# Kernel optimization log

Measured on AMD Instinct MI355X. Metric: run time of the kernel, lower is better.

The kernel has to match this reference:

```python
import jax, jax.numpy as jnp
import numpy as np

N = 100000      # num_nodes
D = 128         # emb_size
LYR = 3         # num_layers
E = 1600000     # num edges (avg degree 16)
Q = 100000      # num label pairs to score


def setup_inputs() -> dict:
    key = jax.random.key(0)
    ks = jax.random.split(key, 8)
    xavier = float(np.sqrt(6.0 / (D + D)))  # xavier_uniform bound for square Linear
    return {
        "edge_index": jax.random.randint(ks[0], (2, E), 0, N),
        "edge_label_index": jax.random.randint(ks[1], (2, Q), 0, N),
        "edge_weight": jax.random.uniform(ks[2], (E,), dtype=jnp.float32),
        "emb": jax.random.uniform(ks[3], (N, D), dtype=jnp.float32, minval=-xavier, maxval=xavier),
        "gc_w": jax.random.uniform(ks[4], (LYR, D, D), dtype=jnp.float32, minval=-xavier, maxval=xavier),
        "gc_b": jnp.zeros((LYR, D), dtype=jnp.float32),
        "bi_w": jax.random.uniform(ks[5], (LYR, D, D), dtype=jnp.float32, minval=-xavier, maxval=xavier),
        "bi_b": jnp.zeros((LYR, D), dtype=jnp.float32),
        "num_nodes": N,
    }


def _get_embedding(edge_index, edge_weight, emb, gc_w, gc_b, bi_w, bi_b, num_nodes):
    row, col = edge_index[0], edge_index[1]
    ego = emb                      # [N, D]
    all_embs = [ego]
    for i in range(gc_w.shape[0]):
        # sparse adj @ ego: out[row] += w * ego[col]
        msg = jax.ops.segment_sum(edge_weight[:, None] * ego[col], row,
                                  num_segments=num_nodes)          # [N, D]
        aggr = msg @ gc_w[i].T + gc_b[i]                            # Linear (torch: x @ W.T + b)
        bi = (ego * msg) @ bi_w[i].T + bi_b[i]
        ego = jax.nn.leaky_relu(aggr + bi, negative_slope=0.2)      # eval mode: dropout = identity
        norm = ego / jnp.maximum(
            jnp.linalg.norm(ego, axis=1, keepdims=True), 1e-12)    # F.normalize(p=2, dim=1)
        all_embs.append(norm)
    return jnp.concatenate(all_embs, axis=1)                        # [N, (L+1)*D]


def reference(edge_index, edge_label_index, edge_weight, emb, gc_w, gc_b, bi_w, bi_b, num_nodes):
    all_embs = _get_embedding(edge_index, edge_weight, emb, gc_w, gc_b, bi_w, bi_b, num_nodes)
    out_src = all_embs[edge_label_index[0]]   # [Q, (L+1)*D]
    out_dst = all_embs[edge_label_index[1]]
    return jnp.sum(out_src * out_dst, axis=-1)  # [Q]
```

## Files before the change

kernel.cpp:

```cpp
#include <hip/hip_runtime.h>

#define DD 128
#define K2 256
#define NBMAX 1024
#define COLMASK 0x01FFFFFF
#define SCAP 4096

typedef short short8 __attribute__((ext_vector_type(8)));
typedef float f32x4  __attribute__((ext_vector_type(4)));

static inline size_t align256(size_t x){ return (x + 255) & ~(size_t)255; }

__device__ __forceinline__ unsigned short f2bf(float x){
  unsigned int u = __builtin_bit_cast(unsigned int, x);
  u += 0x7fff + ((u >> 16) & 1);
  return (unsigned short)(u >> 16);
}
__device__ __forceinline__ float bf2f(unsigned short h){
  unsigned int u = ((unsigned int)h) << 16;
  return __builtin_bit_cast(float, u);
}

__device__ __forceinline__ short8 prod8(short8 mv, short8 ev){
  short8 r;
#pragma unroll
  for (int u = 0; u < 8; u++){
    float p = bf2f((unsigned short)mv[u]) * bf2f((unsigned short)ev[u]);
    r[u] = (short)f2bf(p);
  }
  return r;
}

__global__ __launch_bounds__(256) void bucket_hist_kernel(
    const int* __restrict__ ei, int E, int* __restrict__ bcnt, int NB){
  __shared__ int lh[NBMAX];
  int t = threadIdx.x;
  int base = blockIdx.x * 8192;
  for (int j = t; j < NB; j += 256) lh[j] = 0;
  __syncthreads();
#pragma unroll
  for (int i = 0; i < 32; i++){
    int e = base + i*256 + t;
    if (e < E) atomicAdd(&lh[ei[e] >> 7], 1);
  }
  __syncthreads();
  for (int j = t; j < NB; j += 256){
    int c = lh[j];
    if (c) atomicAdd(&bcnt[j], c);
  }
}

__global__ __launch_bounds__(1024) void bucket_scan_kernel(
    const int* __restrict__ bcnt, int* __restrict__ bbase, int* __restrict__ bcur, int NB){
  __shared__ int a[NBMAX], btmp[NBMAX];
  int t = threadIdx.x;
  a[t] = (t < NB) ? bcnt[t] : 0;
  __syncthreads();
  int* src = a; int* dst = btmp;
  for (int o = 1; o < 1024; o <<= 1){
    int val = src[t];
    if (t >= o) val += src[t - o];
    dst[t] = val;
    __syncthreads();
    int* tm = src; src = dst; dst = tm;
  }
  int excl = (t == 0) ? 0 : src[t-1];
  if (t < NB){ bbase[t] = excl; bcur[t] = excl; }
}

__global__ __launch_bounds__(256) void fill_binned_kernel(
    const int* __restrict__ ei, const float* __restrict__ ew, int E,
    int* __restrict__ bcur, int2* __restrict__ csre, int NB){
  __shared__ int lhist[NBMAX];
  __shared__ int lbase[NBMAX];
  int t = threadIdx.x;
  int base = blockIdx.x * 4096;
  for (int j = t; j < NB; j += 256) lhist[j] = 0;
  __syncthreads();
  int rows[16];
#pragma unroll
  for (int i = 0; i < 16; i++){
    int e = base + i*256 + t;
    int r = (e < E) ? ei[e] : -1;
    rows[i] = r;
    if (r >= 0) atomicAdd(&lhist[r >> 7], 1);
  }
  __syncthreads();
  for (int j = t; j < NB; j += 256){
    int c = lhist[j];
    lbase[j] = c ? atomicAdd(&bcur[j], c) : 0;
    lhist[j] = 0;
  }
  __syncthreads();
#pragma unroll
  for (int i = 0; i < 16; i++){
    int e = base + i*256 + t;
    int r = rows[i];
    if (r >= 0){
      int b = r >> 7;
      int pos = lbase[b] + atomicAdd(&lhist[b], 1);
      int col = ei[E + e];
      float w = ew[e];
      csre[pos] = make_int2(((r & 127) << 25) | col, __float_as_int(w));
    }
  }
}

__global__ __launch_bounds__(256) void bucket_rowdeg_kernel(
    const int* __restrict__ bbase, const int* __restrict__ bcur,
    const int2* __restrict__ csre, int* __restrict__ deg, int* __restrict__ psum, int N){
  __shared__ int lc[128];
  __shared__ int red[128];
  int b = blockIdx.x, t = threadIdx.x;
  if (t < 128) lc[t] = 0;
  __syncthreads();
  int beg = bbase[b], end = bcur[b];
  for (int i = beg + t; i < end; i += 256)
    atomicAdd(&lc[((unsigned int)csre[i].x) >> 25], 1);
  __syncthreads();
  int gr = b*128 + t;
  int d = 0;
  if (t < 128 && gr < N){ d = lc[t]; deg[gr] = d; }
  if (t < 128) red[t] = (d + 7) & ~7;
  __syncthreads();
  for (int o = 64; o > 0; o >>= 1){
    if (t < o) red[t] += red[t+o];
    __syncthreads();
  }
  if (t == 0) psum[b] = red[0];
}

__global__ __launch_bounds__(1024) void pscan_kernel(
    const int* __restrict__ psum, int* __restrict__ pbase, int* __restrict__ rowptrN, int NB){
  __shared__ int a[NBMAX], btmp[NBMAX];
  int t = threadIdx.x;
  a[t] = (t < NB) ? psum[t] : 0;
  __syncthreads();
  int* src = a; int* dst = btmp;
  for (int o = 1; o < 1024; o <<= 1){
    int val = src[t];
    if (t >= o) val += src[t - o];
    dst[t] = val;
    __syncthreads();
    int* tm = src; src = dst; dst = tm;
  }
  int excl = (t == 0) ? 0 : src[t-1];
  if (t < NB) pbase[t] = excl;
  if (t == NB-1) *rowptrN = excl + psum[t];
}

__global__ __launch_bounds__(256) void sortbkt_kernel(
    const int* __restrict__ pbase, const int* __restrict__ bbase, const int* __restrict__ bcur,
    const int* __restrict__ deg, const int2* __restrict__ csre, int2* __restrict__ csre2,
    int* __restrict__ rowptr, int N){
  __shared__ int2 obuf[SCAP];
  __shared__ int lrp[129];
  __shared__ int lcur[128];
  __shared__ int sa[128], sb[128];
  int b = blockIdx.x;
  int t = threadIdx.x;
  int r0 = b*128;
  int gr = r0 + t;
  int d = (t < 128 && gr < N) ? deg[gr] : 0;
  if (t < 128){ sa[t] = (d + 7) & ~7; lcur[t] = 0; }
  __syncthreads();
  int* s0 = sa; int* s1 = sb;
  for (int o = 1; o < 128; o <<= 1){
    if (t < 128){
      int v = s0[t];
      if (t >= o) v += s0[t - o];
      s1[t] = v;
    }
    __syncthreads();
    int* tm = s0; s0 = s1; s1 = tm;
  }
  int pb = pbase[b];
  if (t < 128){
    int excl = t ? s0[t-1] : 0;
    lrp[t] = pb + excl;
    if (gr < N) rowptr[gr] = pb + excl;
    if (t == 127) lrp[128] = pb + s0[127];
  }
  __syncthreads();

  int gb = lrp[0];
  int outLen = lrp[128] - gb;
  int beg = bbase[b], bend = bcur[b];
  const int2 pad = make_int2(0, 0);

  if (outLen <= SCAP){
    for (int i = beg + t; i < bend; i += 256){
      int2 e = csre[i];
      int rl = ((unsigned int)e.x) >> 25;
      int pos = lrp[rl] - gb + atomicAdd(&lcur[rl], 1);
      obuf[pos] = e;
    }
    if (t < 128 && gr < N){
      int pbg = lrp[t] - gb + d, pe = lrp[t+1] - gb;
      for (int i = pbg; i < pe; i++) obuf[i] = pad;
    }
    __syncthreads();
    for (int i = t; i < outLen; i += 256) csre2[gb + i] = obuf[i];
  } else {
    for (int i = beg + t; i < bend; i += 256){
      int2 e = csre[i];
      int rl = ((unsigned int)e.x) >> 25;
      int pos = lrp[rl] + atomicAdd(&lcur[rl], 1);
      csre2[pos] = e;
    }
    __syncthreads();
    if (t < 128 && gr < N){
      int pbeg = lrp[t] + lcur[t];
      int pend = lrp[t+1];
      for (int i = pbeg; i < pend; i++) csre2[i] = pad;
    }
  }
}

__global__ void pack_cvt_kernel(const float* __restrict__ gcw, const float* __restrict__ biw,
                                unsigned short* __restrict__ wb, int LYR,
                                const float* __restrict__ emb, unsigned int* __restrict__ feat4u,
                                int n2, int fsU){
  int i = blockIdx.x*blockDim.x + threadIdx.x;
  int wtotal = LYR*DD*K2;
  if (i < wtotal){
    int l = i / (DD*K2);
    int r = i - l*(DD*K2);
    int n = r >> 8;
    int k = r & (K2-1);
    float v = (k < DD) ? gcw[(size_t)l*DD*DD + n*DD + k]
                       : biw[(size_t)l*DD*DD + n*DD + (k - DD)];
    wb[i] = f2bf(v);
    return;
  }
  int j = i - wtotal;
  if (j < n2){
    float2 v = *(const float2*)(emb + (size_t)j*2);
    int n = j >> 6, c = j & 63;
    feat4u[(size_t)n*fsU + c] = (unsigned int)f2bf(v.x) | ((unsigned int)f2bf(v.y) << 16);
  }
}

__global__ void gather_kernel(const int* __restrict__ rowptr, const int2* __restrict__ csre,
                              const unsigned short* __restrict__ feat, int fs,
                              unsigned int* __restrict__ msgh, int N){
  int wid = (int)(((size_t)blockIdx.x*blockDim.x + threadIdx.x) >> 6);
  int lane = threadIdx.x & 63;
  if (wid >= N) return;
  int beg = rowptr[wid], end = rowptr[wid+1];
  float ax = 0.f, ay = 0.f;
  int k = beg;
  for (; k + 16 <= end; k += 16){
    int2 e[16]; unsigned int v[16];
#pragma unroll
    for (int u = 0; u < 16; u++) e[u] = csre[k+u];
#pragma unroll
    for (int u = 0; u < 16; u++)
      v[u] = *(const unsigned int*)(feat + (size_t)(e[u].x & COLMASK)*fs + lane*2);
#pragma unroll
    for (int u = 0; u < 16; u++){
      float w = __int_as_float(e[u].y);
      ax = fmaf(w, bf2f((unsigned short)v[u]), ax);
      ay = fmaf(w, bf2f((unsigned short)(v[u]>>16)), ay);
    }
  }
  for (; k < end; k += 8){
    int2 e[8]; unsigned int v[8];
#pragma unroll
    for (int u = 0; u < 8; u++) e[u] = csre[k+u];
#pragma unroll
    for (int u = 0; u < 8; u++)
      v[u] = *(const unsigned int*)(feat + (size_t)(e[u].x & COLMASK)*fs + lane*2);
#pragma unroll
    for (int u = 0; u < 8; u++){
      float w = __int_as_float(e[u].y);
      ax = fmaf(w, bf2f((unsigned short)v[u]), ax);
      ay = fmaf(w, bf2f((unsigned short)(v[u]>>16)), ay);
    }
  }
  msgh[(size_t)wid*(DD/2) + lane] = (unsigned int)f2bf(ax) | ((unsigned int)f2bf(ay) << 16);
}

__global__ __launch_bounds__(256) void transform_mfma_kernel(
    const unsigned short* __restrict__ ego_in, const unsigned short* __restrict__ msgh,
    int fs, const unsigned short* __restrict__ wb, const float* __restrict__ gcb,
    const float* __restrict__ bib, unsigned short* __restrict__ ego_out,
    float* __restrict__ nscale, int N){
  int t = threadIdx.x;
  int wave = t >> 6, lane = t & 63;
  int m = lane & 15, q = lane >> 4;
  int wr0 = blockIdx.x * 128 + wave * 32;

  float bias[8];
#pragma unroll
  for (int ct = 0; ct < 8; ct++) bias[ct] = gcb[ct*16 + m] + bib[ct*16 + m];

  int row0 = wr0 + m, row1 = wr0 + 16 + m;
  int cr0 = row0 < N ? row0 : N-1;
  int cr1 = row1 < N ? row1 : N-1;
  const unsigned short* mrow0 = msgh   + (size_t)cr0*DD;
  const unsigned short* mrow1 = msgh   + (size_t)cr1*DD;
  const unsigned short* erow0 = ego_in + (size_t)cr0*fs;
  const unsigned short* erow1 = ego_in + (size_t)cr1*fs;
  const unsigned short* wrow  = wb + (size_t)m*K2;

  f32x4 acc[8][2];
#pragma unroll
  for (int ct = 0; ct < 8; ct++){ acc[ct][0] = (f32x4)0.f; acc[ct][1] = (f32x4)0.f; }

#pragma unroll
  for (int cc = 0; cc < 4; cc++){
    int c = cc*32 + q*8;
    short8 m0 = *(const short8*)(mrow0 + c);
    short8 m1 = *(const short8*)(mrow1 + c);
    short8 e0 = *(const short8*)(erow0 + c);
    short8 e1 = *(const short8*)(erow1 + c);
    short8 p0 = prod8(m0, e0);
    short8 p1 = prod8(m1, e1);
#pragma unroll
    for (int ct = 0; ct < 8; ct++){
      short8 bm = *(const short8*)(wrow + (size_t)ct*16*K2 + c);
      short8 bp = *(const short8*)(wrow + (size_t)ct*16*K2 + DD + c);
      acc[ct][0] = __builtin_amdgcn_mfma_f32_16x16x32_bf16(m0, bm, acc[ct][0], 0, 0, 0);
      acc[ct][1] = __builtin_amdgcn_mfma_f32_16x16x32_bf16(m1, bm, acc[ct][1], 0, 0, 0);
      acc[ct][0] = __builtin_amdgcn_mfma_f32_16x16x32_bf16(p0, bp, acc[ct][0], 0, 0, 0);
      acc[ct][1] = __builtin_amdgcn_mfma_f32_16x16x32_bf16(p1, bp, acc[ct][1], 0, 0, 0);
    }
  }

#pragma unroll
  for (int rt = 0; rt < 2; rt++){
#pragma unroll
    for (int reg = 0; reg < 4; reg++){
      int gr = wr0 + rt*16 + q*4 + reg;
      float rs = 0.f;
#pragma unroll
      for (int ct = 0; ct < 8; ct++){
        float x = acc[ct][rt][reg] + bias[ct];
        x = (x > 0.f) ? x : 0.2f*x;
        rs += x*x;
        if (gr < N) ego_out[(size_t)gr*fs + ct*16 + m] = f2bf(x);
      }
#pragma unroll
      for (int o = 1; o < 16; o <<= 1) rs += __shfl_xor(rs, o, 16);
      if (m == 0 && gr < N)
        nscale[(size_t)gr*3] = 1.0f / fmaxf(sqrtf(rs), 1e-12f);
    }
  }
}

__global__ void score_all_kernel(const int* __restrict__ eli, int Q,
                                 const unsigned int* __restrict__ feat4u, int fsU,
                                 const float* __restrict__ nsall,
                                 float* __restrict__ out){
  int wid = (int)(((size_t)blockIdx.x*blockDim.x + threadIdx.x) >> 6);
  int lane = threadIdx.x & 63;
  if (wid >= Q) return;
  int s = eli[wid];
  int d = eli[Q + wid];
  const unsigned int* sr = feat4u + (size_t)s*fsU + lane;
  const unsigned int* dr = feat4u + (size_t)d*fsU + lane;
  unsigned int a0 = sr[0],   b0 = dr[0];
  unsigned int a1 = sr[64],  b1 = dr[64];
  unsigned int a2 = sr[128], b2 = dr[128];
  unsigned int a3 = sr[192], b3 = dr[192];
  float p0 = bf2f((unsigned short)a0)*bf2f((unsigned short)b0)
           + bf2f((unsigned short)(a0>>16))*bf2f((unsigned short)(b0>>16));
  float p1 = bf2f((unsigned short)a1)*bf2f((unsigned short)b1)
           + bf2f((unsigned short)(a1>>16))*bf2f((unsigned short)(b1>>16));
  float p2 = bf2f((unsigned short)a2)*bf2f((unsigned short)b2)
           + bf2f((unsigned short)(a2>>16))*bf2f((unsigned short)(b2>>16));
  float p3 = bf2f((unsigned short)a3)*bf2f((unsigned short)b3)
           + bf2f((unsigned short)(a3>>16))*bf2f((unsigned short)(b3>>16));
  for (int o = 32; o > 0; o >>= 1){
    p0 += __shfl_xor(p0, o, 64);
    p1 += __shfl_xor(p1, o, 64);
    p2 += __shfl_xor(p2, o, 64);
    p3 += __shfl_xor(p3, o, 64);
  }
  if (lane == 0){
    const float* ss = nsall + (size_t)s*3;
    const float* ds = nsall + (size_t)d*3;
    float r = p0;
    r += p1 * ss[0] * ds[0];
    r += p2 * ss[1] * ds[1];
    r += p3 * ss[2] * ds[2];
    out[wid] = r;
  }
}

extern "C" void kernel_launch(void* const* d_in, const int* in_sizes, int n_in,
                              void* d_out, int out_size, void* d_ws, size_t ws_size,
                              hipStream_t stream){
  const int*   edge_index = (const int*)d_in[0];
  const int*   eli        = (const int*)d_in[1];
  const float* ew         = (const float*)d_in[2];
  const float* emb        = (const float*)d_in[3];
  const float* gcw        = (const float*)d_in[4];
  const float* gcb        = (const float*)d_in[5];
  const float* biw        = (const float*)d_in[6];
  const float* bib        = (const float*)d_in[7];
  const int E   = in_sizes[2];
  const int Q   = in_sizes[1] / 2;
  const int N   = in_sizes[3] / DD;
  const int LYR = in_sizes[4] / (DD*DD);
  float* out = (float*)d_out;

  const int FS  = (LYR + 1) * DD;
  const int FSU = FS / 2;

  char* base = (char*)d_ws;
  size_t off = 0;
  auto carve = [&](size_t bytes)->char*{
    char* r = base + off;
    off = align256(off + bytes);
    return r;
  };

  unsigned short* feat4  = (unsigned short*) carve((size_t)N*FS*sizeof(unsigned short));
  size_t msgB_ = (size_t)N*DD*sizeof(unsigned short);
  size_t csreB_ = (size_t)E*sizeof(int2);
  unsigned short* msgh   = (unsigned short*) carve(msgB_ > csreB_ ? msgB_ : csreB_);
  int2*           csre   = (int2*)msgh;
  unsigned short* wb     = (unsigned short*) carve((size_t)LYR*DD*K2*sizeof(unsigned short));
  float*          nsall  = (float*)          carve((size_t)3*N*sizeof(float));
  int*            rowptr = (int*)            carve((size_t)(N+1)*sizeof(int));
  int*            deg    = (int*)            carve((size_t)N*sizeof(int));
  int*            bcnt   = (int*)            carve((size_t)NBMAX*sizeof(int));
  int*            bbase  = (int*)            carve((size_t)NBMAX*sizeof(int));
  int*            bcur   = (int*)            carve((size_t)NBMAX*sizeof(int));
  int*            psum   = (int*)            carve((size_t)NBMAX*sizeof(int));
  int*            pbase  = (int*)            carve((size_t)NBMAX*sizeof(int));
  int2*           csre2  = (int2*)           carve(((size_t)E + 7*(size_t)N + 8)*sizeof(int2));
  (void)n_in; (void)out_size; (void)ws_size;

  const int NB = (N + 127)/128;

  hipMemsetAsync(bcnt, 0, (size_t)NB*sizeof(int), stream);
  bucket_hist_kernel<<<(E + 8191)/8192, 256, 0, stream>>>(edge_index, E, bcnt, NB);
  bucket_scan_kernel<<<1, 1024, 0, stream>>>(bcnt, bbase, bcur, NB);
  fill_binned_kernel<<<(E + 4095)/4096, 256, 0, stream>>>(edge_index, ew, E, bcur, csre, NB);
  bucket_rowdeg_kernel<<<NB, 256, 0, stream>>>(bbase, bcur, csre, deg, psum, N);
  pscan_kernel<<<1, 1024, 0, stream>>>(psum, pbase, rowptr + N, NB);
  sortbkt_kernel<<<NB, 256, 0, stream>>>(pbase, bbase, bcur, deg, csre, csre2, rowptr, N);
  {
    int total = LYR*DD*K2 + N*DD/2;
    pack_cvt_kernel<<<(total + 255)/256, 256, 0, stream>>>(
        gcw, biw, wb, LYR, emb, (unsigned int*)feat4, N*DD/2, FSU);
  }

  for (int l = 0; l < LYR; l++){
    int blocks = (int)(((size_t)N*64 + 255)/256);
    gather_kernel<<<blocks, 256, 0, stream>>>(rowptr, csre2, feat4 + (size_t)l*DD, FS,
                                              (unsigned int*)msgh, N);
    transform_mfma_kernel<<<(N + 127)/128, 256, 0, stream>>>(
        feat4 + (size_t)l*DD, msgh, FS, wb + (size_t)l*DD*K2,
        gcb + (size_t)l*DD, bib + (size_t)l*DD,
        feat4 + (size_t)(l+1)*DD, nsall + l, N);
  }
  {
    int blocks = (int)(((size_t)Q*64 + 255)/256);
    score_all_kernel<<<blocks, 256, 0, stream>>>(eli, Q, (const unsigned int*)feat4, FSU,
                                                 nsall, out);
  }
}
```

Baseline: 544.4 us.

## Fuse row-degree, scan and bucket sort into one kernel with atomic base

Merges the per-bucket degree count, the global prefix scan and the bucket sort into a single kernel. Each block claims its output range with an atomicAdd on a global cursor, and row ranges are stored as (begin,end) pairs instead of a rowptr array, which removes two launches and the padding of rows to multiples of 8. The gather kernel now handles non-multiple-of-8 tails with a masked final chunk. Bucket order in the CSR becomes nondeterministic, which may reduce locality, and the tail adds a little gather work per row.

```diff
diff --git a/kernel.cpp b/kernel.cpp
--- a/kernel.cpp
+++ b/kernel.cpp
@@ -106,63 +106,24 @@
   }
 }
 
-__global__ __launch_bounds__(256) void bucket_rowdeg_kernel(
+__global__ __launch_bounds__(256) void sortbkt2_kernel(
     const int* __restrict__ bbase, const int* __restrict__ bcur,
-    const int2* __restrict__ csre, int* __restrict__ deg, int* __restrict__ psum, int N){
-  __shared__ int lc[128];
-  __shared__ int red[128];
+    const int2* __restrict__ csre, int2* __restrict__ csre2,
+    int2* __restrict__ rp2, int* __restrict__ gcur, int N){
+  __shared__ int2 obuf[SCAP];
+  __shared__ int lc[128], lcur[128], lrp[128];
+  __shared__ int sa[128], sb[128];
+  __shared__ int gbase;
   int b = blockIdx.x, t = threadIdx.x;
-  if (t < 128) lc[t] = 0;
-  __syncthreads();
-  int beg = bbase[b], end = bcur[b];
-  for (int i = beg + t; i < end; i += 256)
+  int r0 = b*128;
+  if (t < 128){ lc[t] = 0; lcur[t] = 0; }
+  __syncthreads();
+  int beg = bbase[b], bend = bcur[b];
+  for (int i = beg + t; i < bend; i += 256)
     atomicAdd(&lc[((unsigned int)csre[i].x) >> 25], 1);
   __syncthreads();
-  int gr = b*128 + t;
-  int d = 0;
-  if (t < 128 && gr < N){ d = lc[t]; deg[gr] = d; }
-  if (t < 128) red[t] = (d + 7) & ~7;
-  __syncthreads();
-  for (int o = 64; o > 0; o >>= 1){
-    if (t < o) red[t] += red[t+o];
-    __syncthreads();
-  }
-  if (t == 0) psum[b] = red[0];
-}
-
-__global__ __launch_bounds__(1024) void pscan_kernel(
-    const int* __restrict__ psum, int* __restrict__ pbase, int* __restrict__ rowptrN, int NB){
-  __shared__ int a[NBMAX], btmp[NBMAX];
-  int t = threadIdx.x;
-  a[t] = (t < NB) ? psum[t] : 0;
-  __syncthreads();
-  int* src = a; int* dst = btmp;
-  for (int o = 1; o < 1024; o <<= 1){
-    int val = src[t];
-    if (t >= o) val += src[t - o];
-    dst[t] = val;
-    __syncthreads();
-    int* tm = src; src = dst; dst = tm;
-  }
-  int excl = (t == 0) ? 0 : src[t-1];
-  if (t < NB) pbase[t] = excl;
-  if (t == NB-1) *rowptrN = excl + psum[t];
-}
-
-__global__ __launch_bounds__(256) void sortbkt_kernel(
-    const int* __restrict__ pbase, const int* __restrict__ bbase, const int* __restrict__ bcur,
-    const int* __restrict__ deg, const int2* __restrict__ csre, int2* __restrict__ csre2,
-    int* __restrict__ rowptr, int N){
-  __shared__ int2 obuf[SCAP];
-  __shared__ int lrp[129];
-  __shared__ int lcur[128];
-  __shared__ int sa[128], sb[128];
-  int b = blockIdx.x;
-  int t = threadIdx.x;
-  int r0 = b*128;
-  int gr = r0 + t;
-  int d = (t < 128 && gr < N) ? deg[gr] : 0;
-  if (t < 128){ sa[t] = (d + 7) & ~7; lcur[t] = 0; }
+  int d = (t < 128) ? lc[t] : 0;
+  if (t < 128) sa[t] = d;
   __syncthreads();
   int* s0 = sa; int* s1 = sb;
   for (int o = 1; o < 128; o <<= 1){
@@ -174,45 +135,32 @@
     __syncthreads();
     int* tm = s0; s0 = s1; s1 = tm;
   }
-  int pb = pbase[b];
+  int total = s0[127];
+  if (t == 0) gbase = atomicAdd(gcur, total);
+  __syncthreads();
+  int gb = gbase;
   if (t < 128){
     int excl = t ? s0[t-1] : 0;
-    lrp[t] = pb + excl;
-    if (gr < N) rowptr[gr] = pb + excl;
-    if (t == 127) lrp[128] = pb + s0[127];
-  }
-  __syncthreads();
-
-  int gb = lrp[0];
-  int outLen = lrp[128] - gb;
-  int beg = bbase[b], bend = bcur[b];
-  const int2 pad = make_int2(0, 0);
-
-  if (outLen <= SCAP){
+    lrp[t] = excl;
+    int gr = r0 + t;
+    if (gr < N) rp2[gr] = make_int2(gb + excl, gb + excl + d);
+  }
+  __syncthreads();
+  if (total <= SCAP){
     for (int i = beg + t; i < bend; i += 256){
       int2 e = csre[i];
       int rl = ((unsigned int)e.x) >> 25;
-      int pos = lrp[rl] - gb + atomicAdd(&lcur[rl], 1);
+      int pos = lrp[rl] + atomicAdd(&lcur[rl], 1);
       obuf[pos] = e;
     }
-    if (t < 128 && gr < N){
-      int pbg = lrp[t] - gb + d, pe = lrp[t+1] - gb;
-      for (int i = pbg; i < pe; i++) obuf[i] = pad;
-    }
     __syncthreads();
-    for (int i = t; i < outLen; i += 256) csre2[gb + i] = obuf[i];
+    for (int i = t; i < total; i += 256) csre2[gb + i] = obuf[i];
   } else {
     for (int i = beg + t; i < bend; i += 256){
       int2 e = csre[i];
       int rl = ((unsigned int)e.x) >> 25;
-      int pos = lrp[rl] + atomicAdd(&lcur[rl], 1);
+      int pos = gb + lrp[rl] + atomicAdd(&lcur[rl], 1);
       csre2[pos] = e;
-    }
-    __syncthreads();
-    if (t < 128 && gr < N){
-      int pbeg = lrp[t] + lcur[t];
-      int pend = lrp[t+1];
-      for (int i = pbeg; i < pend; i++) csre2[i] = pad;
     }
   }
 }
@@ -241,13 +189,14 @@
   }
 }
 
-__global__ void gather_kernel(const int* __restrict__ rowptr, const int2* __restrict__ csre,
+__global__ void gather_kernel(const int2* __restrict__ rp2, const int2* __restrict__ csre,
                               const unsigned short* __restrict__ feat, int fs,
                               unsigned int* __restrict__ msgh, int N){
   int wid = (int)(((size_t)blockIdx.x*blockDim.x + threadIdx.x) >> 6);
   int lane = threadIdx.x & 63;
   if (wid >= N) return;
-  int beg = rowptr[wid], end = rowptr[wid+1];
+  int2 rp = rp2[wid];
+  int beg = rp.x, end = rp.y;
   float ax = 0.f, ay = 0.f;
   int k = beg;
   for (; k + 16 <= end; k += 16){
@@ -264,10 +213,31 @@
       ay = fmaf(w, bf2f((unsigned short)(v[u]>>16)), ay);
     }
   }
-  for (; k < end; k += 8){
+  for (; k + 8 <= end; k += 8){
     int2 e[8]; unsigned int v[8];
 #pragma unroll
     for (int u = 0; u < 8; u++) e[u] = csre[k+u];
+#pragma unroll
+    for (int u = 0; u < 8; u++)
+      v[u] = *(const unsigned int*)(feat + (size_t)(e[u].x & COLMASK)*fs + lane*2);
+#pragma unroll
+    for (int u = 0; u < 8; u++){
+      float w = __int_as_float(e[u].y);
+      ax = fmaf(w, bf2f((unsigned short)v[u]), ax);
+      ay = fmaf(w, bf2f((unsigned short)(v[u]>>16)), ay);
+    }
+  }
+  if (k < end){
+    int last = end - 1;
+    int2 e[8]; unsigned int v[8];
+#pragma unroll
+    for (int u = 0; u < 8; u++){
+      int idx = k + u;
+      bool ok = idx < end;
+      int2 ee = csre[ok ? idx : last];
+      if (!ok) ee.y = 0;
+      e[u] = ee;
+    }
 #pragma unroll
     for (int u = 0; u < 8; u++)
       v[u] = *(const unsigned int*)(feat + (size_t)(e[u].x & COLMASK)*fs + lane*2);
@@ -424,25 +394,21 @@
   int2*           csre   = (int2*)msgh;
   unsigned short* wb     = (unsigned short*) carve((size_t)LYR*DD*K2*sizeof(unsigned short));
   float*          nsall  = (float*)          carve((size_t)3*N*sizeof(float));
-  int*            rowptr = (int*)            carve((size_t)(N+1)*sizeof(int));
-  int*            deg    = (int*)            carve((size_t)N*sizeof(int));
-  int*            bcnt   = (int*)            carve((size_t)NBMAX*sizeof(int));
+  int2*           rp2    = (int2*)           carve((size_t)N*sizeof(int2));
+  int*            bcnt   = (int*)            carve((size_t)(NBMAX+1)*sizeof(int));
+  int*            gcur   = bcnt + NBMAX;
   int*            bbase  = (int*)            carve((size_t)NBMAX*sizeof(int));
   int*            bcur   = (int*)            carve((size_t)NBMAX*sizeof(int));
-  int*            psum   = (int*)            carve((size_t)NBMAX*sizeof(int));
-  int*            pbase  = (int*)            carve((size_t)NBMAX*sizeof(int));
-  int2*           csre2  = (int2*)           carve(((size_t)E + 7*(size_t)N + 8)*sizeof(int2));
+  int2*           csre2  = (int2*)           carve((size_t)E*sizeof(int2));
   (void)n_in; (void)out_size; (void)ws_size;
 
   const int NB = (N + 127)/128;
 
-  hipMemsetAsync(bcnt, 0, (size_t)NB*sizeof(int), stream);
+  hipMemsetAsync(bcnt, 0, (size_t)(NBMAX+1)*sizeof(int), stream);
   bucket_hist_kernel<<<(E + 8191)/8192, 256, 0, stream>>>(edge_index, E, bcnt, NB);
   bucket_scan_kernel<<<1, 1024, 0, stream>>>(bcnt, bbase, bcur, NB);
   fill_binned_kernel<<<(E + 4095)/4096, 256, 0, stream>>>(edge_index, ew, E, bcur, csre, NB);
-  bucket_rowdeg_kernel<<<NB, 256, 0, stream>>>(bbase, bcur, csre, deg, psum, N);
-  pscan_kernel<<<1, 1024, 0, stream>>>(psum, pbase, rowptr + N, NB);
-  sortbkt_kernel<<<NB, 256, 0, stream>>>(pbase, bbase, bcur, deg, csre, csre2, rowptr, N);
+  sortbkt2_kernel<<<NB, 256, 0, stream>>>(bbase, bcur, csre, csre2, rp2, gcur, N);
   {
     int total = LYR*DD*K2 + N*DD/2;
     pack_cvt_kernel<<<(total + 255)/256, 256, 0, stream>>>(
@@ -451,7 +417,7 @@
 
   for (int l = 0; l < LYR; l++){
     int blocks = (int)(((size_t)N*64 + 255)/256);
-    gather_kernel<<<blocks, 256, 0, stream>>>(rowptr, csre2, feat4 + (size_t)l*DD, FS,
+    gather_kernel<<<blocks, 256, 0, stream>>>(rp2, csre2, feat4 + (size_t)l*DD, FS,
                                               (unsigned int*)msgh, N);
     transform_mfma_kernel<<<(N + 127)/128, 256, 0, stream>>>(
         feat4 + (size_t)l*DD, msgh, FS, wb + (size_t)l*DD*K2,
```

After: 561.5 us. 3.2% more time.
